# Kernel optimization log

Measured on AMD Instinct MI355X. Metric: run time of the kernel, lower is better.

Reference implementation:

```python
import jax, jax.numpy as jnp
import numpy as np

NEG_INF = -9e15


def setup_inputs() -> dict:
    key = jax.random.key(0)
    k1, k2, k3, k4, k5, k6 = jax.random.split(key, 6)
    B, N, F_IN, F_OUT = 16, 2048, 256, 128
    inputs = jax.random.normal(k1, (B, N, F_IN), dtype=jnp.float32)
    adj_matrix = jax.random.randint(k2, (B, N, N), 0, 2, dtype=jnp.int32)
    W = jax.random.normal(k3, (F_OUT, F_IN), dtype=jnp.float32) * (1.0 / np.sqrt(F_IN))
    b_W = jax.random.normal(k4, (F_OUT,), dtype=jnp.float32) * 0.02
    a = jax.random.normal(k5, (1, 2 * F_OUT), dtype=jnp.float32) * (1.0 / np.sqrt(2 * F_OUT))
    b_a = jax.random.normal(k6, (1,), dtype=jnp.float32) * 0.02
    return {"inputs": inputs, "adj_matrix": adj_matrix, "W": W, "b_W": b_W, "a": a, "b_a": b_a}


def reference(inputs, adj_matrix, W, b_W, a, b_a):
    # wh: [B, N, H]
    wh = jnp.einsum('bnf,hf->bnh', inputs, W) + b_W
    H = wh.shape[-1]
    # linear_self_W([wh_i, wh_j]) = a1.wh_i + a2.wh_j + b  (rank-1 linear over concat)
    a1 = a[0, :H]
    a2 = a[0, H:]
    src = jnp.einsum('bnh,h->bn', wh, a1)  # [B, N] contribution of row node i
    dst = jnp.einsum('bnh,h->bn', wh, a2)  # [B, N] contribution of col node j
    e = jax.nn.leaky_relu(src[:, :, None] + dst[:, None, :] + b_a[0], negative_slope=0.01)
    e = jnp.where(adj_matrix > 0, e, NEG_INF)
    att = jax.nn.softmax(e, axis=-1)  # dropout in eval mode = identity
    return jax.nn.elu(jnp.einsum('bij,bjh->bih', att, wh))
```

## Files before the change

kernel.cpp:

```cpp
#include <hip/hip_runtime.h>


#define BDIM 16
#define NDIM 2048
#define FIN 256
#define HDIM 128
#define LOG2E 1.4426950408889634f

typedef short short8 __attribute__((ext_vector_type(8)));
typedef float floatx4 __attribute__((ext_vector_type(4)));

__device__ __forceinline__ unsigned short f2bf(float x) {
    unsigned int u = __float_as_uint(x);
    unsigned int r = (u + 0x7fffu + ((u >> 16) & 1u)) >> 16;
    return (unsigned short)r;
}
__device__ __forceinline__ float bf2f(unsigned short s) {
    return __uint_as_float(((unsigned int)s) << 16);
}

__global__ __launch_bounds__(256) void k_pack(const int* __restrict__ adj,
                                              unsigned* __restrict__ maskG) {
    const int tid = threadIdx.x;
    const int wave = tid >> 6, lane = tid & 63;
    const size_t row0 = (size_t)blockIdx.x * 16 + wave * 4;

    #pragma unroll 1
    for (int r = 0; r < 4; r++) {
        const int* ar = adj + (row0 + r) * NDIM + lane;
        int v[32];
        #pragma unroll
        for (int u = 0; u < 32; u++)
            v[u] = __builtin_nontemporal_load(ar + u * 64);
        unsigned pk[16];
        #pragma unroll
        for (int u = 0; u < 16; u++) {
            unsigned long long b = __ballot(v[u] != 0);
            pk[u] = 0;
            (void)b;
        }
        unsigned lo[32], hi[32];
        #pragma unroll
        for (int u = 0; u < 32; u++) {
            unsigned long long b = __ballot(v[u] != 0);
            lo[u] = (unsigned)b;
            hi[u] = (unsigned)(b >> 32);
        }
        if (lane == 0) {
            unsigned* mo = maskG + (row0 + r) * 64;
            #pragma unroll
            for (int u = 0; u < 16; u++) {
                uint4 o;
                o.x = lo[2 * u];
                o.y = hi[2 * u];
                o.z = lo[2 * u + 1];
                o.w = hi[2 * u + 1];
                *reinterpret_cast<uint4*>(mo + u * 4) = o;
            }
        }
        (void)pk;
    }
}

__global__ __launch_bounds__(256) void k_wh(const float* __restrict__ X,
                                            const float* __restrict__ W,
                                            const float* __restrict__ bW,
                                            const float* __restrict__ a,
                                            const float* __restrict__ ba_p,
                                            float* __restrict__ src,
                                            float* __restrict__ dst,
                                            unsigned short* __restrict__ whF) {
    __shared__ short lds[27648];
    short (*ah)[72] = (short(*)[72])lds;
    short (*al)[72] = (short(*)[72])(lds + 4608);
    short (*bh)[72] = (short(*)[72])(lds + 9216);
    short (*bl)[72] = (short(*)[72])(lds + 18432);
    short (*tb)[72] = (short(*)[72])lds;

    const int tid = threadIdx.x;
    const long row0 = (long)blockIdx.x * 64;
    const int w = tid >> 6, lane = tid & 63;
    const int lm = lane & 15, q = lane >> 4;
    const float ba0 = ba_p[0];

    float a1v[8], a2v[8], bwv[8];
    #pragma unroll
    for (int nt = 0; nt < 8; nt++) {
        a1v[nt] = a[nt * 16 + lm];
        a2v[nt] = a[HDIM + nt * 16 + lm];
        bwv[nt] = bW[nt * 16 + lm];
    }

    floatx4 acc[8];
    #pragma unroll
    for (int nt = 0; nt < 8; nt++) acc[nt] = (floatx4){0.f, 0.f, 0.f, 0.f};

    for (int k0 = 0; k0 < FIN; k0 += 64) {
        #pragma unroll
        for (int u = 0; u < 4; u++) {
            int idx = tid + u * 256;
            int r = idx >> 4, fc = (idx & 15) * 4;
            float4 v = *reinterpret_cast<const float4*>(X + (row0 + r) * FIN + k0 + fc);
            union { unsigned short s[4]; uint2 u2; } ph, pl;
            ph.s[0] = f2bf(v.x); pl.s[0] = f2bf(v.x - bf2f(ph.s[0]));
            ph.s[1] = f2bf(v.y); pl.s[1] = f2bf(v.y - bf2f(ph.s[1]));
            ph.s[2] = f2bf(v.z); pl.s[2] = f2bf(v.z - bf2f(ph.s[2]));
            ph.s[3] = f2bf(v.w); pl.s[3] = f2bf(v.w - bf2f(ph.s[3]));
            *reinterpret_cast<uint2*>(&ah[r][fc]) = ph.u2;
            *reinterpret_cast<uint2*>(&al[r][fc]) = pl.u2;
        }
        #pragma unroll
        for (int u = 0; u < 8; u++) {
            int idx = tid + u * 256;
            int hh = idx >> 4, fc = (idx & 15) * 4;
            float4 v = *reinterpret_cast<const float4*>(W + hh * FIN + k0 + fc);
            union { unsigned short s[4]; uint2 u2; } ph, pl;
            ph.s[0] = f2bf(v.x); pl.s[0] = f2bf(v.x - bf2f(ph.s[0]));
            ph.s[1] = f2bf(v.y); pl.s[1] = f2bf(v.y - bf2f(ph.s[1]));
            ph.s[2] = f2bf(v.z); pl.s[2] = f2bf(v.z - bf2f(ph.s[2]));
            ph.s[3] = f2bf(v.w); pl.s[3] = f2bf(v.w - bf2f(ph.s[3]));
            *reinterpret_cast<uint2*>(&bh[hh][fc]) = ph.u2;
            *reinterpret_cast<uint2*>(&bl[hh][fc]) = pl.u2;
        }
        __syncthreads();
        #pragma unroll
        for (int ks = 0; ks < 64; ks += 32) {
            short8 afh = *reinterpret_cast<const short8*>(&ah[w * 16 + lm][ks + q * 8]);
            short8 afl = *reinterpret_cast<const short8*>(&al[w * 16 + lm][ks + q * 8]);
            #pragma unroll
            for (int nt = 0; nt < 8; nt++) {
                short8 bfh = *reinterpret_cast<const short8*>(&bh[nt * 16 + lm][ks + q * 8]);
                short8 bfl = *reinterpret_cast<const short8*>(&bl[nt * 16 + lm][ks + q * 8]);
                acc[nt] = __builtin_amdgcn_mfma_f32_16x16x32_bf16(afh, bfh, acc[nt], 0, 0, 0);
                acc[nt] = __builtin_amdgcn_mfma_f32_16x16x32_bf16(afh, bfl, acc[nt], 0, 0, 0);
                acc[nt] = __builtin_amdgcn_mfma_f32_16x16x32_bf16(afl, bfh, acc[nt], 0, 0, 0);
            }
        }
        __syncthreads();
    }

    float s1[4] = {0.f, 0.f, 0.f, 0.f}, s2[4] = {0.f, 0.f, 0.f, 0.f};
    #pragma unroll
    for (int nt = 0; nt < 8; nt++) {
        #pragma unroll
        for (int r = 0; r < 4; r++) {
            float v = acc[nt][r] + bwv[nt];
            s1[r] += v * a1v[nt];
            s2[r] += v * a2v[nt];
            tb[nt * 16 + lm][w * 16 + q * 4 + r] = f2bf(v);
        }
    }
    #pragma unroll
    for (int r = 0; r < 4; r++) {
        #pragma unroll
        for (int o = 1; o < 16; o <<= 1) {
            s1[r] += __shfl_xor(s1[r], o);
            s2[r] += __shfl_xor(s2[r], o);
        }
    }
    if (lm == 0) {
        #pragma unroll
        for (int r = 0; r < 4; r++) {
            long row = row0 + w * 16 + q * 4 + r;
            src[row] = (s1[r] + ba0) * LOG2E;
            dst[row] = s2[r] * LOG2E;
        }
    }
    __syncthreads();
    const int b = (int)(row0 >> 11);
    const int jc0 = (int)((row0 & 2047) >> 5);
    const int f = tid >> 4;
    const int sub = tid & 15;
    const int jcrel = f >> 3, ht = f & 7;
    const size_t fbase = (((size_t)b * 64 + jc0 + jcrel) * 8 + ht) * 512;
    #pragma unroll
    for (int i = 0; i < 4; i++) {
        int l = sub * 4 + i;
        uint4 v = *reinterpret_cast<const uint4*>(&tb[ht * 16 + (l & 15)][jcrel * 32 + (l >> 4) * 8]);
        *reinterpret_cast<uint4*>(whF + fbase + l * 8) = v;
    }
}

#define CH(T, PW)                                                              \
    do {                                                                       \
        short8 s0, s1;                                                         \
        if ((T) < 63) {    \
            const unsigned short* gp = gsrc + (size_t)((T) + 1) * 4096;        \
            s0 = *reinterpret_cast<const short8*>(gp);                         \
            s1 = *reinterpret_cast<const short8*>(gp + 512);                   \
            const float* dp = dstp + ((T) + 1) * 32;                           \
            d[(PW) ^ 1][0] = *reinterpret_cast<const floatx4*>(dp);            \
            d[(PW) ^ 1][1] = *reinterpret_cast<const floatx4*>(dp + 4);        \
            md[(PW) ^ 1] = mrow[(T) + 1];                                      \
        }                                                                      \
        const unsigned ms = md[(PW)] >> q8;       \
        short8 af;                                                             \
        _Pragma("unroll")                                                      \
        for (int j = 0; j < 8; j++) {                                          \
            float x = si + d[(PW)][j >> 2][j & 3];                             \
            x = fmaxf(x, 0.01f * x);               \
            float e2 = __builtin_amdgcn_exp2f(x);                              \
            float wgt = (ms & (1u << j)) ? e2 : 0.f;                           \
            lpart += wgt;                                                      \
            af[j] = (short)f2bf(wgt);                                          \
        }                                                                      \
        _Pragma("unroll")                                                      \
        for (int hj = 0; hj < 8; hj++) {                                       \
            short8 fb = *reinterpret_cast<const short8*>(                      \
                &whS[(PW)][hj * 512 + lane * 8]);                              \
            acc[hj] = __builtin_amdgcn_mfma_f32_16x16x32_bf16(af, fb,          \
                                                              acc[hj], 0, 0, 0); \
        }                                                                      \
        if ((T) < 63) {       \
            *reinterpret_cast<short8*>(ldst + ((PW) ^ 1) * 4096) = s0;         \
            *reinterpret_cast<short8*>(ldst + ((PW) ^ 1) * 4096 + 512) = s1;   \
        }                                                                      \
        __syncthreads();                                                       \
    } while (0)

__global__ __launch_bounds__(256) void k_attn(const unsigned* __restrict__ maskG,
                                              const unsigned short* __restrict__ whF,
                                              const float* __restrict__ src,
                                              const float* __restrict__ dst,
                                              float* __restrict__ out) {
    __shared__ short whS[2][4096];
    __shared__ float lred[64];
    __shared__ float linv_s[64];

    const int tid = threadIdx.x;
    const int bid = ((int)blockIdx.x & 7) * 64 + ((int)blockIdx.x >> 3);
    const int b = bid >> 5;
    const int i0 = (bid & 31) * 64;
    const int wave = tid >> 6, lane = tid & 63;
    const int lm = lane & 15, q = lane >> 4;
    const int q8 = q * 8;
    const int irow = i0 + wave * 16 + lm;

    const float si = src[b * NDIM + irow];
    const unsigned* mrow = maskG + (size_t)(b * NDIM + irow) * 64;
    const float* dstp = dst + b * NDIM + q8;
    const unsigned short* gsrc =
        whF + (size_t)b * 64 * 8 * 512 + wave * 1024 + lane * 8;
    short* ldst = &whS[0][0] + wave * 1024 + lane * 8;

    floatx4 acc[8];
    #pragma unroll
    for (int hj = 0; hj < 8; hj++) acc[hj] = (floatx4){0.f, 0.f, 0.f, 0.f};
    float lpart = 0.f;

    unsigned md[2];
    floatx4 d[2][2];

    {
        short8 s0 = *reinterpret_cast<const short8*>(gsrc);
        short8 s1 = *reinterpret_cast<const short8*>(gsrc + 512);
        *reinterpret_cast<short8*>(ldst) = s0;
        *reinterpret_cast<short8*>(ldst + 512) = s1;
    }
    md[0] = mrow[0];
    d[0][0] = *reinterpret_cast<const floatx4*>(dstp);
    d[0][1] = *reinterpret_cast<const floatx4*>(dstp + 4);
    __syncthreads();

    for (int t = 0; t < NDIM / 32; t += 2) {
        CH(t + 0, 0);
        CH(t + 1, 1);
    }

    lpart += __shfl_xor(lpart, 16);
    lpart += __shfl_xor(lpart, 32);
    if (q == 0) lred[wave * 16 + lm] = lpart;
    __syncthreads();
    if (tid < 64) {
        float l = lred[tid];
        linv_s[tid] = l > 0.f ? 1.f / l : 0.f;
    }
    __syncthreads();

    #pragma unroll
    for (int r = 0; r < 4; r++) {
        int il = wave * 16 + q * 4 + r;
        float li = linv_s[il];
        size_t obase = ((size_t)(b * NDIM + i0 + il)) * HDIM + lm;
        #pragma unroll
        for (int hj = 0; hj < 8; hj++) {
            float x = acc[hj][r] * li;
            x = x > 0.f ? x : (__expf(x) - 1.f);
            out[obase + hj * 16] = x;
        }
    }
}

extern "C" void kernel_launch(void* const* d_in, const int* in_sizes, int n_in,
                              void* d_out, int out_size, void* d_ws, size_t ws_size,
                              hipStream_t stream) {
    const float* X  = (const float*)d_in[0];
    const int* adj  = (const int*)d_in[1];
    const float* W  = (const float*)d_in[2];
    const float* bW = (const float*)d_in[3];
    const float* a  = (const float*)d_in[4];
    const float* ba = (const float*)d_in[5];
    float* out = (float*)d_out;

    float* srcv = (float*)d_ws;
    float* dstv = srcv + BDIM * NDIM;
    unsigned short* whF = (unsigned short*)(dstv + BDIM * NDIM);
    unsigned* maskG = (unsigned*)(whF + (size_t)BDIM * NDIM * HDIM);

    k_pack<<<2048, 256, 0, stream>>>(adj, maskG);
    k_wh<<<BDIM * NDIM / 64, 256, 0, stream>>>(X, W, bW, a, ba, srcv, dstv, whF);
    k_attn<<<BDIM * (NDIM / 64), 256, 0, stream>>>(maskG, whF, srcv, dstv, out);
}
```

Before: 430.4 us.

## Fuse adjacency bitmask packing into attention kernel via shared memory

Removes the separate packing kernel. Each attention block now reads its 64 adjacency rows directly, ballots them into a bitmask in shared memory, and then reads mask words from LDS instead of a global packed buffer. This is meant to save the global mask write and read-back plus one kernel launch. The cost is that the large adjacency read is now done by fewer blocks in a serialized prologue before compute, which may reduce achieved memory bandwidth.

```diff
diff --git a/kernel.cpp b/kernel.cpp
--- a/kernel.cpp
+++ b/kernel.cpp
@@ -17,49 +17,6 @@
 }
 __device__ __forceinline__ float bf2f(unsigned short s) {
     return __uint_as_float(((unsigned int)s) << 16);
-}
-
-__global__ __launch_bounds__(256) void k_pack(const int* __restrict__ adj,
-                                              unsigned* __restrict__ maskG) {
-    const int tid = threadIdx.x;
-    const int wave = tid >> 6, lane = tid & 63;
-    const size_t row0 = (size_t)blockIdx.x * 16 + wave * 4;
-
-    #pragma unroll 1
-    for (int r = 0; r < 4; r++) {
-        const int* ar = adj + (row0 + r) * NDIM + lane;
-        int v[32];
-        #pragma unroll
-        for (int u = 0; u < 32; u++)
-            v[u] = __builtin_nontemporal_load(ar + u * 64);
-        unsigned pk[16];
-        #pragma unroll
-        for (int u = 0; u < 16; u++) {
-            unsigned long long b = __ballot(v[u] != 0);
-            pk[u] = 0;
-            (void)b;
-        }
-        unsigned lo[32], hi[32];
-        #pragma unroll
-        for (int u = 0; u < 32; u++) {
-            unsigned long long b = __ballot(v[u] != 0);
-            lo[u] = (unsigned)b;
-            hi[u] = (unsigned)(b >> 32);
-        }
-        if (lane == 0) {
-            unsigned* mo = maskG + (row0 + r) * 64;
-            #pragma unroll
-            for (int u = 0; u < 16; u++) {
-                uint4 o;
-                o.x = lo[2 * u];
-                o.y = hi[2 * u];
-                o.z = lo[2 * u + 1];
-                o.w = hi[2 * u + 1];
-                *reinterpret_cast<uint4*>(mo + u * 4) = o;
-            }
-        }
-        (void)pk;
-    }
 }
 
 __global__ __launch_bounds__(256) void k_wh(const float* __restrict__ X,
@@ -191,7 +148,7 @@
             const float* dp = dstp + ((T) + 1) * 32;                           \
             d[(PW) ^ 1][0] = *reinterpret_cast<const floatx4*>(dp);            \
             d[(PW) ^ 1][1] = *reinterpret_cast<const floatx4*>(dp + 4);        \
-            md[(PW) ^ 1] = mrow[(T) + 1];                                      \
+            md[(PW) ^ 1] = maskS[wrow][(T) + 1];                               \
         }                                                                      \
         const unsigned ms = md[(PW)] >> q8;       \
         short8 af;                                                             \
@@ -218,12 +175,13 @@
         __syncthreads();                                                       \
     } while (0)
 
-__global__ __launch_bounds__(256) void k_attn(const unsigned* __restrict__ maskG,
+__global__ __launch_bounds__(256) void k_attn(const int* __restrict__ adj,
                                               const unsigned short* __restrict__ whF,
                                               const float* __restrict__ src,
                                               const float* __restrict__ dst,
                                               float* __restrict__ out) {
     __shared__ short whS[2][4096];
+    __shared__ unsigned maskS[64][66];
     __shared__ float lred[64];
     __shared__ float linv_s[64];
 
@@ -234,10 +192,32 @@
     const int wave = tid >> 6, lane = tid & 63;
     const int lm = lane & 15, q = lane >> 4;
     const int q8 = q * 8;
-    const int irow = i0 + wave * 16 + lm;
+    const int wrow = wave * 16 + lm;
+    const int irow = i0 + wrow;
+
+    {
+        #pragma unroll 1
+        for (int ri = 0; ri < 16; ri++) {
+            const int lr = wave * 16 + ri;
+            const int* ar = adj + ((size_t)b * NDIM + i0 + lr) * NDIM + lane;
+            int v[32];
+            #pragma unroll
+            for (int u = 0; u < 32; u++)
+                v[u] = __builtin_nontemporal_load(ar + u * 64);
+            #pragma unroll
+            for (int u = 0; u < 32; u++) {
+                unsigned long long bal = __ballot(v[u] != 0);
+                if (lane == 0) {
+                    uint2 pk;
+                    pk.x = (unsigned)bal;
+                    pk.y = (unsigned)(bal >> 32);
+                    *reinterpret_cast<uint2*>(&maskS[lr][2 * u]) = pk;
+                }
+            }
+        }
+    }
 
     const float si = src[b * NDIM + irow];
-    const unsigned* mrow = maskG + (size_t)(b * NDIM + irow) * 64;
     const float* dstp = dst + b * NDIM + q8;
     const unsigned short* gsrc =
         whF + (size_t)b * 64 * 8 * 512 + wave * 1024 + lane * 8;
@@ -257,10 +237,10 @@
         *reinterpret_cast<short8*>(ldst) = s0;
         *reinterpret_cast<short8*>(ldst + 512) = s1;
     }
-    md[0] = mrow[0];
     d[0][0] = *reinterpret_cast<const floatx4*>(dstp);
     d[0][1] = *reinterpret_cast<const floatx4*>(dstp + 4);
     __syncthreads();
+    md[0] = maskS[wrow][0];
 
     for (int t = 0; t < NDIM / 32; t += 2) {
         CH(t + 0, 0);
@@ -305,9 +285,7 @@
     float* srcv = (float*)d_ws;
     float* dstv = srcv + BDIM * NDIM;
     unsigned short* whF = (unsigned short*)(dstv + BDIM * NDIM);
-    unsigned* maskG = (unsigned*)(whF + (size_t)BDIM * NDIM * HDIM);
-
-    k_pack<<<2048, 256, 0, stream>>>(adj, maskG);
+
     k_wh<<<BDIM * NDIM / 64, 256, 0, stream>>>(X, W, bW, a, ba, srcv, dstv, whF);
-    k_attn<<<BDIM * (NDIM / 64), 256, 0, stream>>>(maskG, whF, srcv, dstv, out);
-}
+    k_attn<<<BDIM * (NDIM / 64), 256, 0, stream>>>(adj, whF, srcv, dstv, out);
+}
```

New measurement: 417.5 us. 1.03x faster.
